# Kernel optimization log

Measured on AMD Instinct MI355X. Metric: run time of the kernel, lower is better.

Reference implementation:

```python
import jax, jax.numpy as jnp
import numpy as np

EPS = 1e-3  # Keras BatchNormalization default epsilon
ROWS = 14


def _lstm_step(h, c, x, W, U, b, act):
    # Keras gate order: i, f, g(cell), o
    z = x @ W + h @ U + b
    i, f, g, o = jnp.split(z, 4, axis=-1)
    c = jax.nn.sigmoid(f) * c + jax.nn.sigmoid(i) * act(g)
    h = jax.nn.sigmoid(o) * act(c)
    return h, c


def _lstm(xs, W, U, b, act):
    # xs: [B, T, F] -> (last_h, last_c), zero initial state
    B = xs.shape[0]
    D = U.shape[0]
    h0 = jnp.zeros((B, D), xs.dtype)
    c0 = jnp.zeros((B, D), xs.dtype)

    def step(carry, x):
        h, c = _lstm_step(carry[0], carry[1], x, W, U, b, act)
        return (h, c), h

    (h, c), hs = jax.lax.scan(step, (h0, c0), jnp.swapaxes(xs, 0, 1))
    return jnp.swapaxes(hs, 0, 1), h, c


def _bn(x, gamma, beta):
    # training-mode batchnorm over all axes but the last (channel) axis
    axes = tuple(range(x.ndim - 1))
    mean = jnp.mean(x, axis=axes)
    var = jnp.var(x, axis=axes)
    return (x - mean) * jax.lax.rsqrt(var + EPS) * gamma + beta


def setup_inputs() -> dict:
    key = jax.random.key(0)
    B, T, F = 65536, 32, 16
    D = 8   # lstm_forward_dims = output_dims * 2
    Do = 4  # lstm_backward_dims = output_dims
    ks = jax.random.split(key, 10)
    p = lambda k, shp: (0.1 * jax.random.normal(k, shp)).astype(jnp.float32)
    return {
        "noise_seed": jax.random.normal(ks[0], (B, T, F), dtype=jnp.float32),
        "W0": p(ks[1], (F, 4 * D)), "U0": p(ks[2], (D, 4 * D)), "b0": jnp.zeros((4 * D,), jnp.float32),
        "gamma_h": jnp.ones((D,), jnp.float32), "beta_h": jnp.zeros((D,), jnp.float32),
        "gamma_c": jnp.ones((D,), jnp.float32), "beta_c": jnp.zeros((D,), jnp.float32),
        "W1": p(ks[3], (D, 4 * D)), "U1": p(ks[4], (D, 4 * D)), "b1": jnp.zeros((4 * D,), jnp.float32),
        "gamma3": jnp.ones((D,), jnp.float32), "beta3": jnp.zeros((D,), jnp.float32),
        "W2": p(ks[5], (D, 4 * Do)), "U2": p(ks[6], (Do, 4 * Do)), "b2": jnp.zeros((4 * Do,), jnp.float32),
        "training": 1,
    }


def reference(noise_seed, W0, U0, b0, gamma_h, beta_h, gamma_c, beta_c,
              W1, U1, b1, gamma3, beta3, W2, U2, b2, training):
    # init LSTM (tanh activation), keep final states
    _, h, c = _lstm(noise_seed, W0, U0, b0, jnp.tanh)
    h = _bn(h, gamma_h, beta_h)
    c = _bn(c, gamma_c, beta_c)

    def step(carry, _):
        h, c = carry
        h2, c2 = _lstm_step(h, c, h, W1, U1, b1, jax.nn.relu)
        return (h2, c2), h2

    _, hs = jax.lax.scan(step, (h, c), None, length=ROWS)  # [ROWS, B, D]
    bars = jnp.swapaxes(hs[::-1], 0, 1)                    # reversed, [B, ROWS, D]
    bars = _bn(bars, gamma3, beta3)

    # backward LSTM (relu activation), return_sequences
    out, _, _ = _lstm(bars, W2, U2, b2, jax.nn.relu)       # [B, ROWS, Do]
    return out
```

## Files before the change

kernel.cpp:

```cpp
#include <hip/hip_runtime.h>
#include <hip/hip_bf16.h>

#define EPSV 1e-3f

__device__ __forceinline__ float rcp_fast(float x){ return __builtin_amdgcn_rcpf(x); }
__device__ __forceinline__ float sigm(float x){
    return rcp_fast(1.f + __expf(-x));
}
__device__ __forceinline__ float tanh_fast(float x){
    float e = __expf(2.f * x);
    return 1.f - 2.f * rcp_fast(e + 1.f);
}

template<int K>
__device__ __forceinline__ float bc8(float v){
    return __int_as_float(__builtin_amdgcn_ds_swizzle(__float_as_int(v), (K << 5) | 0x18));
}
#define BC8_ALL(dst, src) do { \
    dst[0]=bc8<0>(src); dst[1]=bc8<1>(src); dst[2]=bc8<2>(src); dst[3]=bc8<3>(src); \
    dst[4]=bc8<4>(src); dst[5]=bc8<5>(src); dst[6]=bc8<6>(src); dst[7]=bc8<7>(src); } while(0)

__global__ __launch_bounds__(256, 2) void k1_lstm0(
    const float* __restrict__ noise, const float* __restrict__ W0,
    const float* __restrict__ U0, const float* __restrict__ b0,
    float* __restrict__ Hbuf, float* __restrict__ Cbuf, double* __restrict__ stats1)
{
    const int tid = threadIdx.x;
    const int d = tid & 7;
    const size_t b = (size_t)blockIdx.x * 32 + (tid >> 3);

    float w0c[16][4], u0c[8][4], b0v[4];
    #pragma unroll
    for (int g = 0; g < 4; ++g) b0v[g] = b0[8*g + d];
    #pragma unroll
    for (int f = 0; f < 16; ++f)
        #pragma unroll
        for (int g = 0; g < 4; ++g) w0c[f][g] = W0[f*32 + 8*g + d];
    #pragma unroll
    for (int e = 0; e < 8; ++e)
        #pragma unroll
        for (int g = 0; g < 4; ++g) u0c[e][g] = U0[e*32 + 8*g + d];

    const float4* __restrict__ xrow = reinterpret_cast<const float4*>(noise + b * 512);
    float h = 0.f, c = 0.f;
    float4 q0 = xrow[0], q1 = xrow[1], q2 = xrow[2], q3 = xrow[3];
    #pragma unroll 2
    for (int t = 0; t < 32; ++t){
        const float x[16] = {q0.x,q0.y,q0.z,q0.w, q1.x,q1.y,q1.z,q1.w,
                             q2.x,q2.y,q2.z,q2.w, q3.x,q3.y,q3.z,q3.w};
        const int tn = (t + 1) & 31;
        q0 = xrow[tn*4+0]; q1 = xrow[tn*4+1]; q2 = xrow[tn*4+2]; q3 = xrow[tn*4+3];
        float hall[8]; BC8_ALL(hall, h);
        float z[4] = {b0v[0], b0v[1], b0v[2], b0v[3]};
        #pragma unroll
        for (int f = 0; f < 16; ++f)
            #pragma unroll
            for (int g = 0; g < 4; ++g) z[g] = fmaf(x[f], w0c[f][g], z[g]);
        #pragma unroll
        for (int e = 0; e < 8; ++e)
            #pragma unroll
            for (int g = 0; g < 4; ++g) z[g] = fmaf(hall[e], u0c[e][g], z[g]);
        c = sigm(z[1])*c + sigm(z[0])*tanh_fast(z[2]);
        h = sigm(z[3])*tanh_fast(c);
    }
    Hbuf[(size_t)blockIdx.x*256 + tid] = h;
    Cbuf[(size_t)blockIdx.x*256 + tid] = c;

    float v0 = h, v1 = h*h, v2 = c, v3 = c*c;
    v0 += __shfl_down(v0,32); v0 += __shfl_down(v0,16); v0 += __shfl_down(v0,8);
    v1 += __shfl_down(v1,32); v1 += __shfl_down(v1,16); v1 += __shfl_down(v1,8);
    v2 += __shfl_down(v2,32); v2 += __shfl_down(v2,16); v2 += __shfl_down(v2,8);
    v3 += __shfl_down(v3,32); v3 += __shfl_down(v3,16); v3 += __shfl_down(v3,8);
    __shared__ float red[4][4][8];
    const int w = tid >> 6;
    if ((tid & 63) < 8){ red[0][w][d]=v0; red[1][w][d]=v1; red[2][w][d]=v2; red[3][w][d]=v3; }
    __syncthreads();
    if (tid < 32){
        const int s = tid >> 3, dd = tid & 7;
        float acc = red[s][0][dd] + red[s][1][dd] + red[s][2][dd] + red[s][3][dd];
        atomicAdd(stats1 + s*8 + dd, (double)acc);
    }
}

__global__ __launch_bounds__(256) void k2_ar(
    const float* __restrict__ Hbuf, const float* __restrict__ Cbuf,
    const double* __restrict__ stats1,
    const float* __restrict__ gamma_h, const float* __restrict__ beta_h,
    const float* __restrict__ gamma_c, const float* __restrict__ beta_c,
    const float* __restrict__ W1, const float* __restrict__ U1, const float* __restrict__ b1,
    double* __restrict__ stats3, int B)
{
    const int tid = threadIdx.x;
    const int d = tid & 7;
    const double invB = 1.0 / (double)B;
    const float meanH = (float)(stats1[d]      * invB);
    const float eH2   = (float)(stats1[8 + d]  * invB);
    const float meanC = (float)(stats1[16 + d] * invB);
    const float eC2   = (float)(stats1[24 + d] * invB);
    const float aH = gamma_h[d] * rsqrtf(eH2 - meanH*meanH + EPSV);
    const float aC = gamma_c[d] * rsqrtf(eC2 - meanC*meanC + EPSV);
    const float bH = beta_h[d] - meanH*aH;
    const float bC = beta_c[d] - meanC*aC;
    float h = fmaf(Hbuf[(size_t)blockIdx.x*256 + tid], aH, bH);
    float c = fmaf(Cbuf[(size_t)blockIdx.x*256 + tid], aC, bC);

    float wc[8][4], bcv[4];
    #pragma unroll
    for (int g = 0; g < 4; ++g) bcv[g] = b1[8*g + d];
    #pragma unroll
    for (int e = 0; e < 8; ++e)
        #pragma unroll
        for (int g = 0; g < 4; ++g) wc[e][g] = W1[e*32 + 8*g + d] + U1[e*32 + 8*g + d];

    float s1 = 0.f, s2 = 0.f;
    #pragma unroll
    for (int r = 0; r < 14; ++r){
        float hall[8]; BC8_ALL(hall, h);
        float z[4] = {bcv[0], bcv[1], bcv[2], bcv[3]};
        #pragma unroll
        for (int e = 0; e < 8; ++e)
            #pragma unroll
            for (int g = 0; g < 4; ++g) z[g] = fmaf(hall[e], wc[e][g], z[g]);
        c = sigm(z[1])*c + sigm(z[0])*fmaxf(z[2], 0.f);
        h = sigm(z[3])*fmaxf(c, 0.f);
        s1 += h; s2 = fmaf(h, h, s2);
    }
    s1 += __shfl_down(s1,32); s1 += __shfl_down(s1,16); s1 += __shfl_down(s1,8);
    s2 += __shfl_down(s2,32); s2 += __shfl_down(s2,16); s2 += __shfl_down(s2,8);
    __shared__ float red[2][4][8];
    const int w = tid >> 6;
    if ((tid & 63) < 8){ red[0][w][d] = s1; red[1][w][d] = s2; }
    __syncthreads();
    if (tid < 16){
        const int s = tid >> 3, dd = tid & 7;
        float acc = red[s][0][dd] + red[s][1][dd] + red[s][2][dd] + red[s][3][dd];
        atomicAdd(stats3 + s*8 + dd, (double)acc);
    }
}

__global__ __launch_bounds__(256, 2) void k3_out(
    const float* __restrict__ Hbuf, const float* __restrict__ Cbuf,
    const double* __restrict__ stats1, const double* __restrict__ stats3,
    const float* __restrict__ gamma_h, const float* __restrict__ beta_h,
    const float* __restrict__ gamma_c, const float* __restrict__ beta_c,
    const float* __restrict__ W1, const float* __restrict__ U1, const float* __restrict__ b1,
    const float* __restrict__ gamma3, const float* __restrict__ beta3,
    const float* __restrict__ W2, const float* __restrict__ U2, const float* __restrict__ b2,
    float* __restrict__ out, int B)
{
    const int tid = threadIdx.x;
    const int d = tid & 7;
    const double invB = 1.0 / (double)B;
    const float meanH = (float)(stats1[d]      * invB);
    const float eH2   = (float)(stats1[8 + d]  * invB);
    const float meanC = (float)(stats1[16 + d] * invB);
    const float eC2   = (float)(stats1[24 + d] * invB);
    const float aH = gamma_h[d] * rsqrtf(eH2 - meanH*meanH + EPSV);
    const float aC = gamma_c[d] * rsqrtf(eC2 - meanC*meanC + EPSV);
    const float bH = beta_h[d] - meanH*aH;
    const float bC = beta_c[d] - meanC*aC;
    float h = fmaf(Hbuf[(size_t)blockIdx.x*256 + tid], aH, bH);
    float c = fmaf(Cbuf[(size_t)blockIdx.x*256 + tid], aC, bC);

    float wc[8][4], bcv[4];
    #pragma unroll
    for (int g = 0; g < 4; ++g) bcv[g] = b1[8*g + d];
    #pragma unroll
    for (int e = 0; e < 8; ++e)
        #pragma unroll
        for (int g = 0; g < 4; ++g) wc[e][g] = W1[e*32 + 8*g + d] + U1[e*32 + 8*g + d];

    float barh[14];
    #pragma unroll
    for (int r = 0; r < 14; ++r){
        float hall[8]; BC8_ALL(hall, h);
        float z[4] = {bcv[0], bcv[1], bcv[2], bcv[3]};
        #pragma unroll
        for (int e = 0; e < 8; ++e)
            #pragma unroll
            for (int g = 0; g < 4; ++g) z[g] = fmaf(hall[e], wc[e][g], z[g]);
        c = sigm(z[1])*c + sigm(z[0])*fmaxf(z[2], 0.f);
        h = sigm(z[3])*fmaxf(c, 0.f);
        barh[r] = h;
    }
    const double invN = 1.0 / ((double)B * 14.0);
    const float mean3 = (float)(stats3[d]     * invN);
    const float e32   = (float)(stats3[8 + d] * invN);
    const float a3 = gamma3[d] * rsqrtf(e32 - mean3*mean3 + EPSV);
    const float b3 = beta3[d] - mean3*a3;
    #pragma unroll
    for (int r = 0; r < 14; ++r) barh[r] = fmaf(barh[r], a3, b3);

    const int q = d & 3;
    float w2c[8][4], u2c[4][4], b2v[4];
    #pragma unroll
    for (int g = 0; g < 4; ++g) b2v[g] = b2[4*g + q];
    #pragma unroll
    for (int e = 0; e < 8; ++e)
        #pragma unroll
        for (int g = 0; g < 4; ++g) w2c[e][g] = W2[e*16 + 4*g + q];
    #pragma unroll
    for (int e = 0; e < 4; ++e)
        #pragma unroll
        for (int g = 0; g < 4; ++g) u2c[e][g] = U2[e*16 + 4*g + q];

    float ho = 0.f, co = 0.f;
    const size_t obase = ((size_t)blockIdx.x*32 + (tid >> 3)) * 56;
    #pragma unroll
    for (int r = 0; r < 14; ++r){
        const float cur = barh[13 - r];
        float be[8]; BC8_ALL(be, cur);
        float h4[4];
        h4[0]=bc8<0>(ho); h4[1]=bc8<1>(ho); h4[2]=bc8<2>(ho); h4[3]=bc8<3>(ho);
        float z[4] = {b2v[0], b2v[1], b2v[2], b2v[3]};
        #pragma unroll
        for (int e = 0; e < 8; ++e)
            #pragma unroll
            for (int g = 0; g < 4; ++g) z[g] = fmaf(be[e], w2c[e][g], z[g]);
        #pragma unroll
        for (int e = 0; e < 4; ++e)
            #pragma unroll
            for (int g = 0; g < 4; ++g) z[g] = fmaf(h4[e], u2c[e][g], z[g]);
        co = sigm(z[1])*co + sigm(z[0])*fmaxf(z[2], 0.f);
        ho = sigm(z[3])*fmaxf(co, 0.f);
        if (d < 4) out[obase + r*4 + d] = ho;
    }
}

extern "C" void kernel_launch(void* const* d_in, const int* in_sizes, int n_in,
                              void* d_out, int out_size, void* d_ws, size_t ws_size,
                              hipStream_t stream)
{
    const float* noise   = (const float*)d_in[0];
    const float* W0      = (const float*)d_in[1];
    const float* U0      = (const float*)d_in[2];
    const float* b0      = (const float*)d_in[3];
    const float* gamma_h = (const float*)d_in[4];
    const float* beta_h  = (const float*)d_in[5];
    const float* gamma_c = (const float*)d_in[6];
    const float* beta_c  = (const float*)d_in[7];
    const float* W1      = (const float*)d_in[8];
    const float* U1      = (const float*)d_in[9];
    const float* b1      = (const float*)d_in[10];
    const float* gamma3  = (const float*)d_in[11];
    const float* beta3   = (const float*)d_in[12];
    const float* W2      = (const float*)d_in[13];
    const float* U2      = (const float*)d_in[14];
    const float* b2      = (const float*)d_in[15];

    const int B = in_sizes[0] / (32 * 16);
    double* stats1 = (double*)d_ws;
    double* stats3 = stats1 + 32;
    float* Hbuf = (float*)((char*)d_ws + 512);
    float* Cbuf = Hbuf + (size_t)B * 8;

    hipMemsetAsync(d_ws, 0, 48 * sizeof(double), stream);
    const int nb = B / 32;
    k1_lstm0<<<nb, 256, 0, stream>>>(noise, W0, U0, b0, Hbuf, Cbuf, stats1);
    k2_ar<<<nb, 256, 0, stream>>>(Hbuf, Cbuf, stats1, gamma_h, beta_h, gamma_c, beta_c,
                                  W1, U1, b1, stats3, B);
    k3_out<<<nb, 256, 0, stream>>>(Hbuf, Cbuf, stats1, stats3, gamma_h, beta_h, gamma_c, beta_c,
                                   W1, U1, b1, gamma3, beta3, W2, U2, b2, (float*)d_out, B);
}
```

Before: 153.7 us.

## Map one batch row per thread with uniform weight loads instead of 8-lane gates

Reworks all three kernels so that each thread owns a whole batch row (all 8 hidden units) and not one hidden unit per lane. The 8-lane swizzle broadcasts go away, and the weights become wave-uniform scalar loads used by a 32-column FMA loop. k3 uses a 64-thread block and stages the normalized bars in LDS for the reverse pass. Each thread now does 8x the FMAs with only 1/8 as many threads, so the aim is to cut cross-lane traffic and per-lane weight registers. In exchange there are far fewer waves and higher register pressure, and each row's 2 KB of noise is read by a single thread, which gives uncoalesced strided loads.

```diff
diff --git a/kernel.cpp b/kernel.cpp
--- a/kernel.cpp
+++ b/kernel.cpp
@@ -4,226 +4,255 @@
 #define EPSV 1e-3f
 
 __device__ __forceinline__ float rcp_fast(float x){ return __builtin_amdgcn_rcpf(x); }
-__device__ __forceinline__ float sigm(float x){
-    return rcp_fast(1.f + __expf(-x));
-}
+__device__ __forceinline__ float sigm(float x){ return rcp_fast(1.f + __expf(-x)); }
 __device__ __forceinline__ float tanh_fast(float x){
     float e = __expf(2.f * x);
     return 1.f - 2.f * rcp_fast(e + 1.f);
 }
-
-template<int K>
-__device__ __forceinline__ float bc8(float v){
-    return __int_as_float(__builtin_amdgcn_ds_swizzle(__float_as_int(v), (K << 5) | 0x18));
-}
-#define BC8_ALL(dst, src) do { \
-    dst[0]=bc8<0>(src); dst[1]=bc8<1>(src); dst[2]=bc8<2>(src); dst[3]=bc8<3>(src); \
-    dst[4]=bc8<4>(src); dst[5]=bc8<5>(src); dst[6]=bc8<6>(src); dst[7]=bc8<7>(src); } while(0)
-
-__global__ __launch_bounds__(256, 2) void k1_lstm0(
-    const float* __restrict__ noise, const float* __restrict__ W0,
-    const float* __restrict__ U0, const float* __restrict__ b0,
-    float* __restrict__ Hbuf, float* __restrict__ Cbuf, double* __restrict__ stats1)
+__device__ __forceinline__ float wave_sum(float v){
+    v += __shfl_xor(v, 1);  v += __shfl_xor(v, 2);  v += __shfl_xor(v, 4);
+    v += __shfl_xor(v, 8);  v += __shfl_xor(v, 16); v += __shfl_xor(v, 32);
+    return v;
+}
+
+__global__ __launch_bounds__(256)
+__attribute__((amdgpu_waves_per_eu(1, 4)))
+void k1_lstm0(const float* __restrict__ noise, const float* __restrict__ W0,
+              const float* __restrict__ U0, const float* __restrict__ b0,
+              float* __restrict__ Hbuf, float* __restrict__ Cbuf,
+              double* __restrict__ stats1)
 {
     const int tid = threadIdx.x;
-    const int d = tid & 7;
-    const size_t b = (size_t)blockIdx.x * 32 + (tid >> 3);
-
-    float w0c[16][4], u0c[8][4], b0v[4];
-    #pragma unroll
-    for (int g = 0; g < 4; ++g) b0v[g] = b0[8*g + d];
-    #pragma unroll
-    for (int f = 0; f < 16; ++f)
-        #pragma unroll
-        for (int g = 0; g < 4; ++g) w0c[f][g] = W0[f*32 + 8*g + d];
-    #pragma unroll
-    for (int e = 0; e < 8; ++e)
-        #pragma unroll
-        for (int g = 0; g < 4; ++g) u0c[e][g] = U0[e*32 + 8*g + d];
-
-    const float4* __restrict__ xrow = reinterpret_cast<const float4*>(noise + b * 512);
-    float h = 0.f, c = 0.f;
-    float4 q0 = xrow[0], q1 = xrow[1], q2 = xrow[2], q3 = xrow[3];
-    #pragma unroll 2
+    const size_t s = (size_t)blockIdx.x * 256 + tid;
+    const float4* __restrict__ xr = reinterpret_cast<const float4*>(noise + s * 512);
+
+    float h[8], c[8];
+    #pragma unroll
+    for (int u = 0; u < 8; ++u){ h[u] = 0.f; c[u] = 0.f; }
+
+    float4 p0 = xr[0], p1 = xr[1], p2 = xr[2], p3 = xr[3];
+
+    #pragma unroll 1
     for (int t = 0; t < 32; ++t){
-        const float x[16] = {q0.x,q0.y,q0.z,q0.w, q1.x,q1.y,q1.z,q1.w,
-                             q2.x,q2.y,q2.z,q2.w, q3.x,q3.y,q3.z,q3.w};
+        const float x[16] = {p0.x,p0.y,p0.z,p0.w, p1.x,p1.y,p1.z,p1.w,
+                             p2.x,p2.y,p2.z,p2.w, p3.x,p3.y,p3.z,p3.w};
         const int tn = (t + 1) & 31;
-        q0 = xrow[tn*4+0]; q1 = xrow[tn*4+1]; q2 = xrow[tn*4+2]; q3 = xrow[tn*4+3];
-        float hall[8]; BC8_ALL(hall, h);
-        float z[4] = {b0v[0], b0v[1], b0v[2], b0v[3]};
-        #pragma unroll
-        for (int f = 0; f < 16; ++f)
-            #pragma unroll
-            for (int g = 0; g < 4; ++g) z[g] = fmaf(x[f], w0c[f][g], z[g]);
-        #pragma unroll
-        for (int e = 0; e < 8; ++e)
-            #pragma unroll
-            for (int g = 0; g < 4; ++g) z[g] = fmaf(hall[e], u0c[e][g], z[g]);
-        c = sigm(z[1])*c + sigm(z[0])*tanh_fast(z[2]);
-        h = sigm(z[3])*tanh_fast(c);
-    }
-    Hbuf[(size_t)blockIdx.x*256 + tid] = h;
-    Cbuf[(size_t)blockIdx.x*256 + tid] = c;
-
-    float v0 = h, v1 = h*h, v2 = c, v3 = c*c;
-    v0 += __shfl_down(v0,32); v0 += __shfl_down(v0,16); v0 += __shfl_down(v0,8);
-    v1 += __shfl_down(v1,32); v1 += __shfl_down(v1,16); v1 += __shfl_down(v1,8);
-    v2 += __shfl_down(v2,32); v2 += __shfl_down(v2,16); v2 += __shfl_down(v2,8);
-    v3 += __shfl_down(v3,32); v3 += __shfl_down(v3,16); v3 += __shfl_down(v3,8);
-    __shared__ float red[4][4][8];
-    const int w = tid >> 6;
-    if ((tid & 63) < 8){ red[0][w][d]=v0; red[1][w][d]=v1; red[2][w][d]=v2; red[3][w][d]=v3; }
+        p0 = xr[tn*4+0]; p1 = xr[tn*4+1]; p2 = xr[tn*4+2]; p3 = xr[tn*4+3];
+
+        float z[32];
+        #pragma unroll
+        for (int col = 0; col < 32; ++col) z[col] = b0[col];
+        #pragma unroll
+        for (int f = 0; f < 16; ++f){
+            const float xv = x[f];
+            #pragma unroll
+            for (int col = 0; col < 32; ++col) z[col] = fmaf(xv, W0[f*32 + col], z[col]);
+        }
+        #pragma unroll
+        for (int e = 0; e < 8; ++e){
+            const float hv = h[e];
+            #pragma unroll
+            for (int col = 0; col < 32; ++col) z[col] = fmaf(hv, U0[e*32 + col], z[col]);
+        }
+        #pragma unroll
+        for (int u = 0; u < 8; ++u){
+            c[u] = fmaf(sigm(z[8+u]), c[u], sigm(z[u]) * tanh_fast(z[16+u]));
+            h[u] = sigm(z[24+u]) * tanh_fast(c[u]);
+        }
+    }
+
+    float4* Hv = reinterpret_cast<float4*>(Hbuf + s * 8);
+    float4* Cv = reinterpret_cast<float4*>(Cbuf + s * 8);
+    Hv[0] = make_float4(h[0],h[1],h[2],h[3]); Hv[1] = make_float4(h[4],h[5],h[6],h[7]);
+    Cv[0] = make_float4(c[0],c[1],c[2],c[3]); Cv[1] = make_float4(c[4],c[5],c[6],c[7]);
+
+    __shared__ float red[4][32];
+    const int wv = tid >> 6, ln = tid & 63;
+    #pragma unroll
+    for (int u = 0; u < 8; ++u){
+        const float a0 = wave_sum(h[u]);
+        const float a1 = wave_sum(h[u]*h[u]);
+        const float a2 = wave_sum(c[u]);
+        const float a3 = wave_sum(c[u]*c[u]);
+        if (ln == 0){ red[wv][u] = a0; red[wv][8+u] = a1; red[wv][16+u] = a2; red[wv][24+u] = a3; }
+    }
     __syncthreads();
     if (tid < 32){
-        const int s = tid >> 3, dd = tid & 7;
-        float acc = red[s][0][dd] + red[s][1][dd] + red[s][2][dd] + red[s][3][dd];
-        atomicAdd(stats1 + s*8 + dd, (double)acc);
-    }
-}
-
-__global__ __launch_bounds__(256) void k2_ar(
-    const float* __restrict__ Hbuf, const float* __restrict__ Cbuf,
-    const double* __restrict__ stats1,
-    const float* __restrict__ gamma_h, const float* __restrict__ beta_h,
-    const float* __restrict__ gamma_c, const float* __restrict__ beta_c,
-    const float* __restrict__ W1, const float* __restrict__ U1, const float* __restrict__ b1,
-    double* __restrict__ stats3, int B)
+        const float acc = red[0][tid] + red[1][tid] + red[2][tid] + red[3][tid];
+        atomicAdd(stats1 + tid, (double)acc);
+    }
+}
+
+__global__ __launch_bounds__(256)
+__attribute__((amdgpu_waves_per_eu(1, 4)))
+void k2_ar(const float* __restrict__ Hbuf, const float* __restrict__ Cbuf,
+           const double* __restrict__ stats1,
+           const float* __restrict__ gamma_h, const float* __restrict__ beta_h,
+           const float* __restrict__ gamma_c, const float* __restrict__ beta_c,
+           const float* __restrict__ W1, const float* __restrict__ U1,
+           const float* __restrict__ b1, double* __restrict__ stats3, int B)
 {
     const int tid = threadIdx.x;
-    const int d = tid & 7;
+    const size_t s = (size_t)blockIdx.x * 256 + tid;
+
+    float h[8], c[8];
+    {
+        const float4* Hv = reinterpret_cast<const float4*>(Hbuf + s * 8);
+        const float4* Cv = reinterpret_cast<const float4*>(Cbuf + s * 8);
+        float4 a = Hv[0], b = Hv[1], d = Cv[0], e = Cv[1];
+        h[0]=a.x;h[1]=a.y;h[2]=a.z;h[3]=a.w; h[4]=b.x;h[5]=b.y;h[6]=b.z;h[7]=b.w;
+        c[0]=d.x;c[1]=d.y;c[2]=d.z;c[3]=d.w; c[4]=e.x;c[5]=e.y;c[6]=e.z;c[7]=e.w;
+    }
     const double invB = 1.0 / (double)B;
-    const float meanH = (float)(stats1[d]      * invB);
-    const float eH2   = (float)(stats1[8 + d]  * invB);
-    const float meanC = (float)(stats1[16 + d] * invB);
-    const float eC2   = (float)(stats1[24 + d] * invB);
-    const float aH = gamma_h[d] * rsqrtf(eH2 - meanH*meanH + EPSV);
-    const float aC = gamma_c[d] * rsqrtf(eC2 - meanC*meanC + EPSV);
-    const float bH = beta_h[d] - meanH*aH;
-    const float bC = beta_c[d] - meanC*aC;
-    float h = fmaf(Hbuf[(size_t)blockIdx.x*256 + tid], aH, bH);
-    float c = fmaf(Cbuf[(size_t)blockIdx.x*256 + tid], aC, bC);
-
-    float wc[8][4], bcv[4];
-    #pragma unroll
-    for (int g = 0; g < 4; ++g) bcv[g] = b1[8*g + d];
-    #pragma unroll
-    for (int e = 0; e < 8; ++e)
-        #pragma unroll
-        for (int g = 0; g < 4; ++g) wc[e][g] = W1[e*32 + 8*g + d] + U1[e*32 + 8*g + d];
-
-    float s1 = 0.f, s2 = 0.f;
-    #pragma unroll
+    #pragma unroll
+    for (int u = 0; u < 8; ++u){
+        const float mH = (float)(stats1[u]      * invB);
+        const float eH = (float)(stats1[8 + u]  * invB);
+        const float mC = (float)(stats1[16 + u] * invB);
+        const float eC = (float)(stats1[24 + u] * invB);
+        const float aH = gamma_h[u] * rsqrtf(eH - mH*mH + EPSV);
+        const float aC = gamma_c[u] * rsqrtf(eC - mC*mC + EPSV);
+        h[u] = fmaf(h[u], aH, beta_h[u] - mH*aH);
+        c[u] = fmaf(c[u], aC, beta_c[u] - mC*aC);
+    }
+
+    float s1[8], s2[8];
+    #pragma unroll
+    for (int u = 0; u < 8; ++u){ s1[u] = 0.f; s2[u] = 0.f; }
+
+    #pragma unroll 1
     for (int r = 0; r < 14; ++r){
-        float hall[8]; BC8_ALL(hall, h);
-        float z[4] = {bcv[0], bcv[1], bcv[2], bcv[3]};
-        #pragma unroll
-        for (int e = 0; e < 8; ++e)
-            #pragma unroll
-            for (int g = 0; g < 4; ++g) z[g] = fmaf(hall[e], wc[e][g], z[g]);
-        c = sigm(z[1])*c + sigm(z[0])*fmaxf(z[2], 0.f);
-        h = sigm(z[3])*fmaxf(c, 0.f);
-        s1 += h; s2 = fmaf(h, h, s2);
-    }
-    s1 += __shfl_down(s1,32); s1 += __shfl_down(s1,16); s1 += __shfl_down(s1,8);
-    s2 += __shfl_down(s2,32); s2 += __shfl_down(s2,16); s2 += __shfl_down(s2,8);
-    __shared__ float red[2][4][8];
-    const int w = tid >> 6;
-    if ((tid & 63) < 8){ red[0][w][d] = s1; red[1][w][d] = s2; }
+        float z[32];
+        #pragma unroll
+        for (int col = 0; col < 32; ++col) z[col] = b1[col];
+        #pragma unroll
+        for (int e = 0; e < 8; ++e){
+            const float hv = h[e];
+            #pragma unroll
+            for (int col = 0; col < 32; ++col) z[col] = fmaf(hv, W1[e*32 + col], z[col]);
+            #pragma unroll
+            for (int col = 0; col < 32; ++col) z[col] = fmaf(hv, U1[e*32 + col], z[col]);
+        }
+        #pragma unroll
+        for (int u = 0; u < 8; ++u){
+            c[u] = fmaf(sigm(z[8+u]), c[u], sigm(z[u]) * fmaxf(z[16+u], 0.f));
+            h[u] = sigm(z[24+u]) * fmaxf(c[u], 0.f);
+            s1[u] += h[u]; s2[u] = fmaf(h[u], h[u], s2[u]);
+        }
+    }
+
+    __shared__ float red[4][16];
+    const int wv = tid >> 6, ln = tid & 63;
+    #pragma unroll
+    for (int u = 0; u < 8; ++u){
+        const float a0 = wave_sum(s1[u]);
+        const float a1 = wave_sum(s2[u]);
+        if (ln == 0){ red[wv][u] = a0; red[wv][8+u] = a1; }
+    }
     __syncthreads();
     if (tid < 16){
-        const int s = tid >> 3, dd = tid & 7;
-        float acc = red[s][0][dd] + red[s][1][dd] + red[s][2][dd] + red[s][3][dd];
-        atomicAdd(stats3 + s*8 + dd, (double)acc);
-    }
-}
-
-__global__ __launch_bounds__(256, 2) void k3_out(
-    const float* __restrict__ Hbuf, const float* __restrict__ Cbuf,
-    const double* __restrict__ stats1, const double* __restrict__ stats3,
-    const float* __restrict__ gamma_h, const float* __restrict__ beta_h,
-    const float* __restrict__ gamma_c, const float* __restrict__ beta_c,
-    const float* __restrict__ W1, const float* __restrict__ U1, const float* __restrict__ b1,
-    const float* __restrict__ gamma3, const float* __restrict__ beta3,
-    const float* __restrict__ W2, const float* __restrict__ U2, const float* __restrict__ b2,
-    float* __restrict__ out, int B)
-{
+        const float acc = red[0][tid] + red[1][tid] + red[2][tid] + red[3][tid];
+        atomicAdd(stats3 + tid, (double)acc);
+    }
+}
+
+__global__ __launch_bounds__(64)
+__attribute__((amdgpu_waves_per_eu(1, 4)))
+void k3_out(const float* __restrict__ Hbuf, const float* __restrict__ Cbuf,
+            const double* __restrict__ stats1, const double* __restrict__ stats3,
+            const float* __restrict__ gamma_h, const float* __restrict__ beta_h,
+            const float* __restrict__ gamma_c, const float* __restrict__ beta_c,
+            const float* __restrict__ W1, const float* __restrict__ U1,
+            const float* __restrict__ b1,
+            const float* __restrict__ gamma3, const float* __restrict__ beta3,
+            const float* __restrict__ W2, const float* __restrict__ U2,
+            const float* __restrict__ b2, float* __restrict__ out, int B)
+{
+    __shared__ float bars[14][8][64];
     const int tid = threadIdx.x;
-    const int d = tid & 7;
+    const size_t s = (size_t)blockIdx.x * 64 + tid;
+
+    float h[8], c[8];
+    {
+        const float4* Hv = reinterpret_cast<const float4*>(Hbuf + s * 8);
+        const float4* Cv = reinterpret_cast<const float4*>(Cbuf + s * 8);
+        float4 a = Hv[0], b = Hv[1], d = Cv[0], e = Cv[1];
+        h[0]=a.x;h[1]=a.y;h[2]=a.z;h[3]=a.w; h[4]=b.x;h[5]=b.y;h[6]=b.z;h[7]=b.w;
+        c[0]=d.x;c[1]=d.y;c[2]=d.z;c[3]=d.w; c[4]=e.x;c[5]=e.y;c[6]=e.z;c[7]=e.w;
+    }
     const double invB = 1.0 / (double)B;
-    const float meanH = (float)(stats1[d]      * invB);
-    const float eH2   = (float)(stats1[8 + d]  * invB);
-    const float meanC = (float)(stats1[16 + d] * invB);
-    const float eC2   = (float)(stats1[24 + d] * invB);
-    const float aH = gamma_h[d] * rsqrtf(eH2 - meanH*meanH + EPSV);
-    const float aC = gamma_c[d] * rsqrtf(eC2 - meanC*meanC + EPSV);
-    const float bH = beta_h[d] - meanH*aH;
-    const float bC = beta_c[d] - meanC*aC;
-    float h = fmaf(Hbuf[(size_t)blockIdx.x*256 + tid], aH, bH);
-    float c = fmaf(Cbuf[(size_t)blockIdx.x*256 + tid], aC, bC);
-
-    float wc[8][4], bcv[4];
-    #pragma unroll
-    for (int g = 0; g < 4; ++g) bcv[g] = b1[8*g + d];
-    #pragma unroll
-    for (int e = 0; e < 8; ++e)
-        #pragma unroll
-        for (int g = 0; g < 4; ++g) wc[e][g] = W1[e*32 + 8*g + d] + U1[e*32 + 8*g + d];
-
-    float barh[14];
-    #pragma unroll
+    #pragma unroll
+    for (int u = 0; u < 8; ++u){
+        const float mH = (float)(stats1[u]      * invB);
+        const float eH = (float)(stats1[8 + u]  * invB);
+        const float mC = (float)(stats1[16 + u] * invB);
+        const float eC = (float)(stats1[24 + u] * invB);
+        const float aH = gamma_h[u] * rsqrtf(eH - mH*mH + EPSV);
+        const float aC = gamma_c[u] * rsqrtf(eC - mC*mC + EPSV);
+        h[u] = fmaf(h[u], aH, beta_h[u] - mH*aH);
+        c[u] = fmaf(c[u], aC, beta_c[u] - mC*aC);
+    }
+    const double invN = 1.0 / ((double)B * 14.0);
+    float a3[8], b3[8];
+    #pragma unroll
+    for (int u = 0; u < 8; ++u){
+        const float m3 = (float)(stats3[u]     * invN);
+        const float e3 = (float)(stats3[8 + u] * invN);
+        a3[u] = gamma3[u] * rsqrtf(e3 - m3*m3 + EPSV);
+        b3[u] = beta3[u] - m3*a3[u];
+    }
+
+    #pragma unroll 1
     for (int r = 0; r < 14; ++r){
-        float hall[8]; BC8_ALL(hall, h);
-        float z[4] = {bcv[0], bcv[1], bcv[2], bcv[3]};
-        #pragma unroll
-        for (int e = 0; e < 8; ++e)
-            #pragma unroll
-            for (int g = 0; g < 4; ++g) z[g] = fmaf(hall[e], wc[e][g], z[g]);
-        c = sigm(z[1])*c + sigm(z[0])*fmaxf(z[2], 0.f);
-        h = sigm(z[3])*fmaxf(c, 0.f);
-        barh[r] = h;
-    }
-    const double invN = 1.0 / ((double)B * 14.0);
-    const float mean3 = (float)(stats3[d]     * invN);
-    const float e32   = (float)(stats3[8 + d] * invN);
-    const float a3 = gamma3[d] * rsqrtf(e32 - mean3*mean3 + EPSV);
-    const float b3 = beta3[d] - mean3*a3;
-    #pragma unroll
-    for (int r = 0; r < 14; ++r) barh[r] = fmaf(barh[r], a3, b3);
-
-    const int q = d & 3;
-    float w2c[8][4], u2c[4][4], b2v[4];
-    #pragma unroll
-    for (int g = 0; g < 4; ++g) b2v[g] = b2[4*g + q];
-    #pragma unroll
-    for (int e = 0; e < 8; ++e)
-        #pragma unroll
-        for (int g = 0; g < 4; ++g) w2c[e][g] = W2[e*16 + 4*g + q];
-    #pragma unroll
-    for (int e = 0; e < 4; ++e)
-        #pragma unroll
-        for (int g = 0; g < 4; ++g) u2c[e][g] = U2[e*16 + 4*g + q];
-
-    float ho = 0.f, co = 0.f;
-    const size_t obase = ((size_t)blockIdx.x*32 + (tid >> 3)) * 56;
-    #pragma unroll
-    for (int r = 0; r < 14; ++r){
-        const float cur = barh[13 - r];
-        float be[8]; BC8_ALL(be, cur);
-        float h4[4];
-        h4[0]=bc8<0>(ho); h4[1]=bc8<1>(ho); h4[2]=bc8<2>(ho); h4[3]=bc8<3>(ho);
-        float z[4] = {b2v[0], b2v[1], b2v[2], b2v[3]};
-        #pragma unroll
-        for (int e = 0; e < 8; ++e)
-            #pragma unroll
-            for (int g = 0; g < 4; ++g) z[g] = fmaf(be[e], w2c[e][g], z[g]);
-        #pragma unroll
-        for (int e = 0; e < 4; ++e)
-            #pragma unroll
-            for (int g = 0; g < 4; ++g) z[g] = fmaf(h4[e], u2c[e][g], z[g]);
-        co = sigm(z[1])*co + sigm(z[0])*fmaxf(z[2], 0.f);
-        ho = sigm(z[3])*fmaxf(co, 0.f);
-        if (d < 4) out[obase + r*4 + d] = ho;
+        float z[32];
+        #pragma unroll
+        for (int col = 0; col < 32; ++col) z[col] = b1[col];
+        #pragma unroll
+        for (int e = 0; e < 8; ++e){
+            const float hv = h[e];
+            #pragma unroll
+            for (int col = 0; col < 32; ++col) z[col] = fmaf(hv, W1[e*32 + col], z[col]);
+            #pragma unroll
+            for (int col = 0; col < 32; ++col) z[col] = fmaf(hv, U1[e*32 + col], z[col]);
+        }
+        #pragma unroll
+        for (int u = 0; u < 8; ++u){
+            c[u] = fmaf(sigm(z[8+u]), c[u], sigm(z[u]) * fmaxf(z[16+u], 0.f));
+            h[u] = sigm(z[24+u]) * fmaxf(c[u], 0.f);
+            bars[r][u][tid] = fmaf(h[u], a3[u], b3[u]);
+        }
+    }
+
+    float ho[4], co[4];
+    #pragma unroll
+    for (int u = 0; u < 4; ++u){ ho[u] = 0.f; co[u] = 0.f; }
+    #pragma unroll 1
+    for (int i = 0; i < 14; ++i){
+        const int r = 13 - i;
+        float be[8];
+        #pragma unroll
+        for (int e = 0; e < 8; ++e) be[e] = bars[r][e][tid];
+        float z2[16];
+        #pragma unroll
+        for (int col = 0; col < 16; ++col) z2[col] = b2[col];
+        #pragma unroll
+        for (int e = 0; e < 8; ++e){
+            const float bv = be[e];
+            #pragma unroll
+            for (int col = 0; col < 16; ++col) z2[col] = fmaf(bv, W2[e*16 + col], z2[col]);
+        }
+        #pragma unroll
+        for (int e = 0; e < 4; ++e){
+            const float hv = ho[e];
+            #pragma unroll
+            for (int col = 0; col < 16; ++col) z2[col] = fmaf(hv, U2[e*16 + col], z2[col]);
+        }
+        #pragma unroll
+        for (int u = 0; u < 4; ++u){
+            co[u] = fmaf(sigm(z2[4+u]), co[u], sigm(z2[u]) * fmaxf(z2[8+u], 0.f));
+            ho[u] = sigm(z2[12+u]) * fmaxf(co[u], 0.f);
+        }
+        *reinterpret_cast<float4*>(out + s*56 + i*4) = make_float4(ho[0],ho[1],ho[2],ho[3]);
     }
 }
 
@@ -255,10 +284,10 @@
     float* Cbuf = Hbuf + (size_t)B * 8;
 
     hipMemsetAsync(d_ws, 0, 48 * sizeof(double), stream);
-    const int nb = B / 32;
-    k1_lstm0<<<nb, 256, 0, stream>>>(noise, W0, U0, b0, Hbuf, Cbuf, stats1);
-    k2_ar<<<nb, 256, 0, stream>>>(Hbuf, Cbuf, stats1, gamma_h, beta_h, gamma_c, beta_c,
-                                  W1, U1, b1, stats3, B);
-    k3_out<<<nb, 256, 0, stream>>>(Hbuf, Cbuf, stats1, stats3, gamma_h, beta_h, gamma_c, beta_c,
-                                   W1, U1, b1, gamma3, beta3, W2, U2, b2, (float*)d_out, B);
-}
+    k1_lstm0<<<B/256, 256, 0, stream>>>(noise, W0, U0, b0, Hbuf, Cbuf, stats1);
+    k2_ar  <<<B/256, 256, 0, stream>>>(Hbuf, Cbuf, stats1, gamma_h, beta_h, gamma_c, beta_c,
+                                       W1, U1, b1, stats3, B);
+    k3_out <<<B/64, 64, 0, stream>>>(Hbuf, Cbuf, stats1, stats3, gamma_h, beta_h,
+                                     gamma_c, beta_c, W1, U1, b1, gamma3, beta3,
+                                     W2, U2, b2, (float*)d_out, B);
+}
```

Measured after the change: 226.1 us. +47.1%, slower.

## Split LSTM0 gates across 16 lanes per sample and pin weights in registers

Applied to the files above, without the earlier changes.

The first LSTM kernel now gives each sample 16 lanes instead of 8, so each lane computes two gate pre-activations rather than four. The i/g and f/o pairs are recombined with a lane swizzle, and one sigmoid/tanh formula is chosen per lane by coefficients. The input prefetch is dropped and the time loop is no longer unrolled. Empty asm barriers pin weight arrays in registers, and waves-per-EU hints are added to k1 and k3. The aim is a shorter per-sample dependency chain and more parallelism, at the cost of each sample's input row being loaded redundantly by 16 lanes and twice as many blocks.

```diff
diff --git a/kernel.cpp b/kernel.cpp
--- a/kernel.cpp
+++ b/kernel.cpp
@@ -4,14 +4,17 @@
 #define EPSV 1e-3f
 
 __device__ __forceinline__ float rcp_fast(float x){ return __builtin_amdgcn_rcpf(x); }
-__device__ __forceinline__ float sigm(float x){
-    return rcp_fast(1.f + __expf(-x));
-}
+__device__ __forceinline__ float sigm(float x){ return rcp_fast(1.f + __expf(-x)); }
 __device__ __forceinline__ float tanh_fast(float x){
     float e = __expf(2.f * x);
     return 1.f - 2.f * rcp_fast(e + 1.f);
 }
-
+#define KEEP(x) asm volatile("" : "+v"(x))
+
+template<int OR, int AND>
+__device__ __forceinline__ float swz(float v){
+    return __int_as_float(__builtin_amdgcn_ds_swizzle(__float_as_int(v), (OR << 5) | AND));
+}
 template<int K>
 __device__ __forceinline__ float bc8(float v){
     return __int_as_float(__builtin_amdgcn_ds_swizzle(__float_as_int(v), (K << 5) | 0x18));
@@ -19,66 +22,76 @@
 #define BC8_ALL(dst, src) do { \
     dst[0]=bc8<0>(src); dst[1]=bc8<1>(src); dst[2]=bc8<2>(src); dst[3]=bc8<3>(src); \
     dst[4]=bc8<4>(src); dst[5]=bc8<5>(src); dst[6]=bc8<6>(src); dst[7]=bc8<7>(src); } while(0)
-
-__global__ __launch_bounds__(256, 2) void k1_lstm0(
-    const float* __restrict__ noise, const float* __restrict__ W0,
-    const float* __restrict__ U0, const float* __restrict__ b0,
-    float* __restrict__ Hbuf, float* __restrict__ Cbuf, double* __restrict__ stats1)
+#define BCAST16(dst, src) do { \
+    dst[0]=swz<0,0x10>(src); dst[1]=swz<1,0x10>(src); dst[2]=swz<2,0x10>(src); dst[3]=swz<3,0x10>(src); \
+    dst[4]=swz<4,0x10>(src); dst[5]=swz<5,0x10>(src); dst[6]=swz<6,0x10>(src); dst[7]=swz<7,0x10>(src); } while(0)
+
+__global__ __launch_bounds__(256)
+__attribute__((amdgpu_waves_per_eu(2, 4)))
+void k1_lstm0(const float* __restrict__ noise, const float* __restrict__ W0,
+              const float* __restrict__ U0, const float* __restrict__ b0,
+              float* __restrict__ Hbuf, float* __restrict__ Cbuf,
+              double* __restrict__ stats1)
 {
     const int tid = threadIdx.x;
-    const int d = tid & 7;
-    const size_t b = (size_t)blockIdx.x * 32 + (tid >> 3);
-
-    float w0c[16][4], u0c[8][4], b0v[4];
-    #pragma unroll
-    for (int g = 0; g < 4; ++g) b0v[g] = b0[8*g + d];
-    #pragma unroll
-    for (int f = 0; f < 16; ++f)
-        #pragma unroll
-        for (int g = 0; g < 4; ++g) w0c[f][g] = W0[f*32 + 8*g + d];
-    #pragma unroll
-    for (int e = 0; e < 8; ++e)
-        #pragma unroll
-        for (int g = 0; g < 4; ++g) u0c[e][g] = U0[e*32 + 8*g + d];
-
-    const float4* __restrict__ xrow = reinterpret_cast<const float4*>(noise + b * 512);
-    float h = 0.f, c = 0.f;
-    float4 q0 = xrow[0], q1 = xrow[1], q2 = xrow[2], q3 = xrow[3];
-    #pragma unroll 2
+    const int l = tid & 15;
+    const size_t s = (size_t)blockIdx.x * 16 + (tid >> 4);
+
+    float wa[16], wb[16], ua[8], ub[8];
+    #pragma unroll
+    for (int f = 0; f < 16; ++f){ wa[f] = W0[f*32 + l]; wb[f] = W0[f*32 + l + 16]; }
+    #pragma unroll
+    for (int e = 0; e < 8; ++e){ ua[e] = U0[e*32 + l]; ub[e] = U0[e*32 + l + 16]; }
+    float ba = b0[l], bb = b0[l + 16];
+    #pragma unroll
+    for (int f = 0; f < 16; ++f){ KEEP(wa[f]); KEEP(wb[f]); }
+    #pragma unroll
+    for (int e = 0; e < 8; ++e){ KEEP(ua[e]); KEEP(ub[e]); }
+    KEEP(ba); KEEP(bb);
+
+    const float k1s = (l < 8) ? -2.f : -1.f;
+    const float m1  = (l < 8) ?  2.f :  1.f;
+    const float n1  = (l < 8) ? -1.f :  0.f;
+
+    const float4* __restrict__ xr = reinterpret_cast<const float4*>(noise + s * 512);
+
+    float h = 0.f, c = 0.f, hall[8];
+    #pragma unroll
+    for (int e = 0; e < 8; ++e) hall[e] = 0.f;
+
+    #pragma unroll 1
     for (int t = 0; t < 32; ++t){
-        const float x[16] = {q0.x,q0.y,q0.z,q0.w, q1.x,q1.y,q1.z,q1.w,
-                             q2.x,q2.y,q2.z,q2.w, q3.x,q3.y,q3.z,q3.w};
-        const int tn = (t + 1) & 31;
-        q0 = xrow[tn*4+0]; q1 = xrow[tn*4+1]; q2 = xrow[tn*4+2]; q3 = xrow[tn*4+3];
-        float hall[8]; BC8_ALL(hall, h);
-        float z[4] = {b0v[0], b0v[1], b0v[2], b0v[3]};
-        #pragma unroll
-        for (int f = 0; f < 16; ++f)
-            #pragma unroll
-            for (int g = 0; g < 4; ++g) z[g] = fmaf(x[f], w0c[f][g], z[g]);
-        #pragma unroll
-        for (int e = 0; e < 8; ++e)
-            #pragma unroll
-            for (int g = 0; g < 4; ++g) z[g] = fmaf(hall[e], u0c[e][g], z[g]);
-        c = sigm(z[1])*c + sigm(z[0])*tanh_fast(z[2]);
-        h = sigm(z[3])*tanh_fast(c);
-    }
-    Hbuf[(size_t)blockIdx.x*256 + tid] = h;
-    Cbuf[(size_t)blockIdx.x*256 + tid] = c;
+        float4 p0 = xr[t*4+0], p1 = xr[t*4+1], p2 = xr[t*4+2], p3 = xr[t*4+3];
+        float z0 = ba, z1 = bb;
+        #pragma unroll
+        for (int e = 0; e < 8; ++e){ z0 = fmaf(hall[e], ua[e], z0); z1 = fmaf(hall[e], ub[e], z1); }
+        const float x[16] = {p0.x,p0.y,p0.z,p0.w, p1.x,p1.y,p1.z,p1.w,
+                             p2.x,p2.y,p2.z,p2.w, p3.x,p3.y,p3.z,p3.w};
+        #pragma unroll
+        for (int f = 0; f < 16; ++f){ z0 = fmaf(x[f], wa[f], z0); z1 = fmaf(x[f], wb[f], z1); }
+        const float a0 = sigm(z0);
+        const float a1 = fmaf(rcp_fast(1.f + __expf(z1 * k1s)), m1, n1);
+        const float fv = swz<8, 0x17>(a0);
+        const float ov = swz<8, 0x17>(a1);
+        c = fmaf(fv, c, a0 * a1);
+        h = ov * tanh_fast(c);
+        BCAST16(hall, h);
+    }
+
+    if (l < 8){ Hbuf[s*8 + l] = h; Cbuf[s*8 + l] = c; }
 
     float v0 = h, v1 = h*h, v2 = c, v3 = c*c;
-    v0 += __shfl_down(v0,32); v0 += __shfl_down(v0,16); v0 += __shfl_down(v0,8);
-    v1 += __shfl_down(v1,32); v1 += __shfl_down(v1,16); v1 += __shfl_down(v1,8);
-    v2 += __shfl_down(v2,32); v2 += __shfl_down(v2,16); v2 += __shfl_down(v2,8);
-    v3 += __shfl_down(v3,32); v3 += __shfl_down(v3,16); v3 += __shfl_down(v3,8);
-    __shared__ float red[4][4][8];
-    const int w = tid >> 6;
-    if ((tid & 63) < 8){ red[0][w][d]=v0; red[1][w][d]=v1; red[2][w][d]=v2; red[3][w][d]=v3; }
+    v0 += __shfl_xor(v0,16); v0 += __shfl_xor(v0,32);
+    v1 += __shfl_xor(v1,16); v1 += __shfl_xor(v1,32);
+    v2 += __shfl_xor(v2,16); v2 += __shfl_xor(v2,32);
+    v3 += __shfl_xor(v3,16); v3 += __shfl_xor(v3,32);
+    __shared__ float red[4][32];
+    const int wv = tid >> 6, ln = tid & 63;
+    if (ln < 8){ red[wv][ln] = v0; red[wv][8+ln] = v1; red[wv][16+ln] = v2; red[wv][24+ln] = v3; }
     __syncthreads();
     if (tid < 32){
-        const int s = tid >> 3, dd = tid & 7;
-        float acc = red[s][0][dd] + red[s][1][dd] + red[s][2][dd] + red[s][3][dd];
-        atomicAdd(stats1 + s*8 + dd, (double)acc);
+        const float acc = red[0][tid] + red[1][tid] + red[2][tid] + red[3][tid];
+        atomicAdd(stats1 + tid, (double)acc);
     }
 }
 
@@ -99,10 +112,8 @@
     const float eC2   = (float)(stats1[24 + d] * invB);
     const float aH = gamma_h[d] * rsqrtf(eH2 - meanH*meanH + EPSV);
     const float aC = gamma_c[d] * rsqrtf(eC2 - meanC*meanC + EPSV);
-    const float bH = beta_h[d] - meanH*aH;
-    const float bC = beta_c[d] - meanC*aC;
-    float h = fmaf(Hbuf[(size_t)blockIdx.x*256 + tid], aH, bH);
-    float c = fmaf(Cbuf[(size_t)blockIdx.x*256 + tid], aC, bC);
+    float h = fmaf(Hbuf[(size_t)blockIdx.x*256 + tid], aH, beta_h[d] - meanH*aH);
+    float c = fmaf(Cbuf[(size_t)blockIdx.x*256 + tid], aC, beta_c[d] - meanC*aC);
 
     float wc[8][4], bcv[4];
     #pragma unroll
@@ -132,13 +143,15 @@
     if ((tid & 63) < 8){ red[0][w][d] = s1; red[1][w][d] = s2; }
     __syncthreads();
     if (tid < 16){
-        const int s = tid >> 3, dd = tid & 7;
-        float acc = red[s][0][dd] + red[s][1][dd] + red[s][2][dd] + red[s][3][dd];
-        atomicAdd(stats3 + s*8 + dd, (double)acc);
-    }
-}
-
-__global__ __launch_bounds__(256, 2) void k3_out(
+        const int st = tid >> 3, dd = tid & 7;
+        float acc = red[st][0][dd] + red[st][1][dd] + red[st][2][dd] + red[st][3][dd];
+        atomicAdd(stats3 + st*8 + dd, (double)acc);
+    }
+}
+
+__global__ __launch_bounds__(256)
+__attribute__((amdgpu_waves_per_eu(2, 2)))
+void k3_out(
     const float* __restrict__ Hbuf, const float* __restrict__ Cbuf,
     const double* __restrict__ stats1, const double* __restrict__ stats3,
     const float* __restrict__ gamma_h, const float* __restrict__ beta_h,
@@ -157,10 +170,8 @@
     const float eC2   = (float)(stats1[24 + d] * invB);
     const float aH = gamma_h[d] * rsqrtf(eH2 - meanH*meanH + EPSV);
     const float aC = gamma_c[d] * rsqrtf(eC2 - meanC*meanC + EPSV);
-    const float bH = beta_h[d] - meanH*aH;
-    const float bC = beta_c[d] - meanC*aC;
-    float h = fmaf(Hbuf[(size_t)blockIdx.x*256 + tid], aH, bH);
-    float c = fmaf(Cbuf[(size_t)blockIdx.x*256 + tid], aC, bC);
+    float h = fmaf(Hbuf[(size_t)blockIdx.x*256 + tid], aH, beta_h[d] - meanH*aH);
+    float c = fmaf(Cbuf[(size_t)blockIdx.x*256 + tid], aC, beta_c[d] - meanC*aC);
 
     float wc[8][4], bcv[4];
     #pragma unroll
@@ -169,6 +180,10 @@
     for (int e = 0; e < 8; ++e)
         #pragma unroll
         for (int g = 0; g < 4; ++g) wc[e][g] = W1[e*32 + 8*g + d] + U1[e*32 + 8*g + d];
+    #pragma unroll
+    for (int e = 0; e < 8; ++e)
+        #pragma unroll
+        for (int g = 0; g < 4; ++g) KEEP(wc[e][g]);
 
     float barh[14];
     #pragma unroll
@@ -203,6 +218,14 @@
     for (int e = 0; e < 4; ++e)
         #pragma unroll
         for (int g = 0; g < 4; ++g) u2c[e][g] = U2[e*16 + 4*g + q];
+    #pragma unroll
+    for (int e = 0; e < 8; ++e)
+        #pragma unroll
+        for (int g = 0; g < 4; ++g) KEEP(w2c[e][g]);
+    #pragma unroll
+    for (int e = 0; e < 4; ++e)
+        #pragma unroll
+        for (int g = 0; g < 4; ++g) KEEP(u2c[e][g]);
 
     float ho = 0.f, co = 0.f;
     const size_t obase = ((size_t)blockIdx.x*32 + (tid >> 3)) * 56;
@@ -255,10 +278,10 @@
     float* Cbuf = Hbuf + (size_t)B * 8;
 
     hipMemsetAsync(d_ws, 0, 48 * sizeof(double), stream);
-    const int nb = B / 32;
-    k1_lstm0<<<nb, 256, 0, stream>>>(noise, W0, U0, b0, Hbuf, Cbuf, stats1);
-    k2_ar<<<nb, 256, 0, stream>>>(Hbuf, Cbuf, stats1, gamma_h, beta_h, gamma_c, beta_c,
-                                  W1, U1, b1, stats3, B);
-    k3_out<<<nb, 256, 0, stream>>>(Hbuf, Cbuf, stats1, stats3, gamma_h, beta_h, gamma_c, beta_c,
-                                   W1, U1, b1, gamma3, beta3, W2, U2, b2, (float*)d_out, B);
-}
+    k1_lstm0<<<B/16, 256, 0, stream>>>(noise, W0, U0, b0, Hbuf, Cbuf, stats1);
+    k2_ar  <<<B/32, 256, 0, stream>>>(Hbuf, Cbuf, stats1, gamma_h, beta_h, gamma_c, beta_c,
+                                      W1, U1, b1, stats3, B);
+    k3_out <<<B/32, 256, 0, stream>>>(Hbuf, Cbuf, stats1, stats3, gamma_h, beta_h,
+                                      gamma_c, beta_c, W1, U1, b1, gamma3, beta3,
+                                      W2, U2, b2, (float*)d_out, B);
+}
```

Result: slower. 188.8 us (+22.8%).
